# Kernel optimization log

Measured on AMD Instinct MI355X. Metric: run time of the kernel, lower is better.

## Reference

```python
import jax, jax.numpy as jnp
import numpy as np

EPS = 1e-8  # matches F.cosine_similarity default eps


def setup_inputs() -> dict:
    key = jax.random.key(0)
    k1, k2, k3 = jax.random.split(key, 3)
    B, C, H, W = 16, 256, 64, 64
    n_e = 1024
    z = jax.random.normal(k1, (B, C, H, W), dtype=jnp.float32)
    gt = jax.random.normal(k2, (B, C, H, W), dtype=jnp.float32)
    codebook = jax.random.normal(k3, (n_e, C), dtype=jnp.float32)
    return {"z": z, "gt": gt, "codebook": codebook}


def _sq_dist(x, cb):
    return (jnp.sum(x * x, axis=1, keepdims=True)
            + jnp.sum(cb * cb, axis=1)
            - 2.0 * x @ cb.T)


def reference(z, gt, codebook):
    B, C, H, W = z.shape
    # permute to (B,H,W,C) then flatten to (N, e_dim)
    zf = jnp.transpose(z, (0, 2, 3, 1)).reshape(-1, C)
    gf = jnp.transpose(gt, (0, 2, 3, 1)).reshape(-1, C)

    idx = jnp.argmin(_sq_dist(zf, codebook), axis=1)       # [N]
    idx_gt = jnp.argmin(_sq_dist(gf, codebook), axis=1)    # [N]

    # one-hot @ codebook == direct gather
    z_q = codebook[idx].reshape(B, H, W, C)
    z_q_gt = codebook[idx_gt].reshape(B, H, W, C)

    # F.cosine_similarity(z_q_gt, z_q, dim=1) on (B,H,W,C): reduces over H -> (B,W,C)
    num = jnp.sum(z_q_gt * z_q, axis=1)
    nx = jnp.maximum(jnp.sqrt(jnp.sum(z_q_gt * z_q_gt, axis=1)), EPS)
    ny = jnp.maximum(jnp.sqrt(jnp.sum(z_q * z_q, axis=1)), EPS)
    cosine_score = num / (nx * ny)                         # (B, W, C)

    return cosine_score, idx_gt[:, None], idx[:, None]
```

## Files before the change

kernel.cpp:

```cpp
#include <hip/hip_runtime.h>

typedef _Float16 f16x8 __attribute__((ext_vector_type(8)));
typedef float f32x4 __attribute__((ext_vector_type(4)));

#define CDIM 256
#define NE 1024
#define HW 4096
#define CHW 1048576
#define OUT_COS 262144
#define N_PIX 65536
#define NT 32
#define TAU 0.1f


__global__ void prep_kernel(const float* __restrict__ cb,
                            _Float16* __restrict__ hi,
                            float* __restrict__ c2f,
                            double* __restrict__ c2d) {
    int code = blockIdx.x;
    int lane = threadIdx.x;
    int t = code >> 5, sub = (code >> 4) & 1, n = code & 15;
    const float* row = cb + code * CDIM;
    double s = 0.0;
    #pragma unroll
    for (int i = 0; i < 4; ++i) {
        int d = i * 64 + lane;
        float x = row[d];
        s += (double)x * (double)x;
        int f = d >> 5, q = (d >> 3) & 3, r = d & 7;
        hi[(size_t)t * 8192 + sub * 4096 + f * 512 + q * 128 + n * 8 + r] =
            (_Float16)x;
    }
    #pragma unroll
    for (int off = 32; off > 0; off >>= 1)
        s += __shfl_down(s, off, 64);
    if (lane == 0) { c2f[code] = (float)(0.5 * s); c2d[code] = 0.5 * s; }
}

__device__ __forceinline__ void gl_lds16(const _Float16* g, _Float16* l) {
    __builtin_amdgcn_global_load_lds(
        (const __attribute__((address_space(1))) unsigned int*)g,
        (__attribute__((address_space(3))) unsigned int*)l, 16, 0, 0);
}

__attribute__((amdgpu_waves_per_eu(2, 2)))
__launch_bounds__(256)
__global__ void argmin_kernel(const float* __restrict__ Z,
                              const float* __restrict__ GT,
                              const _Float16* __restrict__ ghi,
                              const float* __restrict__ cb,
                              const float* __restrict__ c2f,
                              const double* __restrict__ c2d,
                              float* __restrict__ out_z,
                              float* __restrict__ out_gt) {
    __shared__ __align__(16) _Float16 lbuf[2][8192];
    __shared__ int cand_lds[4][64];
    __shared__ float c2s[NE];
    const int wave = threadIdx.x >> 6;
    const int lane = threadIdx.x & 63;
    const int l15 = lane & 15;
    const int quad = lane >> 4;
    const int half = blockIdx.x >> 8;
    const float* X = half ? GT : Z;
    float* out_idx = half ? out_gt : out_z;
    const int p0 = (blockIdx.x & 255) * 256;

    #pragma unroll
    for (int i = 0; i < 4; ++i)
        c2s[i * 256 + threadIdx.x] = c2f[i * 256 + threadIdx.x];

    f16x8 nah[4][8];
    #pragma unroll
    for (int g = 0; g < 4; ++g) {
        const int p = p0 + wave * 64 + g * 16 + l15;
        const float* xbase = X + (size_t)(p >> 12) * CHW + (p & 4095);
        #pragma unroll
        for (int f = 0; f < 8; ++f) {
            #pragma unroll
            for (int j = 0; j < 8; ++j) {
                int d = f * 32 + quad * 8 + j;
                nah[g][f][j] = -(_Float16)xbase[(size_t)d * HW];
            }
        }
    }

    int b1[4][4], b2[4][4];
    #pragma unroll
    for (int g = 0; g < 4; ++g)
        #pragma unroll
        for (int r = 0; r < 4; ++r) { b1[g][r] = 0x7fffffff; b2[g][r] = 0x7fffffff; }

    auto stage = [&](int b, int t) {
        #pragma unroll
        for (int i = 0; i < 4; ++i) {
            const int c = wave * 4 + i;
            gl_lds16(ghi + (size_t)t * 8192 + c * 512 + lane * 8, &lbuf[b][c * 512]);
        }
    };

    stage(0, 0);
    __syncthreads();

    for (int t = 0; t < NT; ++t) {
        const int cur = t & 1;
        if (t < NT - 1) stage(cur ^ 1, t + 1);

        #pragma unroll
        for (int sub = 0; sub < 2; ++sub) {
            const int n = t * 32 + sub * 16 + l15;
            const float c2 = c2s[n];
            f32x4 acc[4];
            #pragma unroll
            for (int g = 0; g < 4; ++g)
                acc[g] = (f32x4){c2, c2, c2, c2};

            #pragma unroll
            for (int f = 0; f < 8; ++f) {
                f16x8 bh = *(const f16x8*)&lbuf[cur][sub * 4096 + f * 512 + lane * 8];
                acc[0] = __builtin_amdgcn_mfma_f32_16x16x32_f16(nah[0][f], bh, acc[0], 0, 0, 0);
                acc[1] = __builtin_amdgcn_mfma_f32_16x16x32_f16(nah[1][f], bh, acc[1], 0, 0, 0);
                acc[2] = __builtin_amdgcn_mfma_f32_16x16x32_f16(nah[2][f], bh, acc[2], 0, 0, 0);
                acc[3] = __builtin_amdgcn_mfma_f32_16x16x32_f16(nah[3][f], bh, acc[3], 0, 0, 0);
            }

            #pragma unroll
            for (int g = 0; g < 4; ++g) {
                #pragma unroll
                for (int r = 0; r < 4; ++r) {
                    int k = (__float_as_int(acc[g][r]) & 0xFFFFFC00) | n;
                    int mx = max(b1[g][r], k);
                    b2[g][r] = min(b2[g][r], mx);
                    b1[g][r] = min(b1[g][r], k);
                }
            }
        }
        __syncthreads();
    }

    #pragma unroll
    for (int g = 0; g < 4; ++g) {
        #pragma unroll
        for (int r = 0; r < 4; ++r) {
            int x1 = b1[g][r], x2 = b2[g][r];
            #pragma unroll
            for (int off = 8; off > 0; off >>= 1) {
                int o1 = __shfl_xor(x1, off, 64);
                int o2 = __shfl_xor(x2, off, 64);
                int tt = max(x1, o1);
                x2 = min(min(x2, o2), tt);
                x1 = min(x1, o1);
            }
            if (l15 == 0) {
                const int i1 = x1 & 1023, i2 = x2 & 1023;
                const float s1 = __int_as_float(x1 & 0xFFFFFC00);
                const float s2 = __int_as_float(x2 & 0xFFFFFC00);
                const int row = quad * 4 + r;
                const int slot = g * 16 + row;
                const bool flag = (s2 - s1) < TAU;
                cand_lds[wave][slot] = i1 | (i2 << 10) | (flag ? (1 << 20) : 0);
                if (!flag) out_idx[p0 + wave * 64 + slot] = (float)i1;
            }
        }
    }

    const int info = cand_lds[wave][lane];
    if (info & (1 << 20)) {
        const int i1 = info & 1023, i2 = (info >> 10) & 1023;
        const int p = p0 + wave * 64 + lane;
        const float* xb = X + (size_t)(p >> 12) * CHW + (p & 4095);
        const float* r1 = cb + (size_t)i1 * CDIM;
        const float* r2 = cb + (size_t)i2 * CDIM;
        double d1 = 0.0, d2 = 0.0;
        #pragma unroll 4
        for (int d = 0; d < CDIM; d += 4) {
            float x0 = xb[(size_t)(d + 0) * HW];
            float x1v = xb[(size_t)(d + 1) * HW];
            float x2v = xb[(size_t)(d + 2) * HW];
            float x3v = xb[(size_t)(d + 3) * HW];
            const float4 v1 = *(const float4*)(r1 + d);
            const float4 v2 = *(const float4*)(r2 + d);
            d1 += (double)x0 * v1.x + (double)x1v * v1.y
                + (double)x2v * v1.z + (double)x3v * v1.w;
            d2 += (double)x0 * v2.x + (double)x1v * v2.y
                + (double)x2v * v2.z + (double)x3v * v2.w;
        }
        const double dd1 = c2d[i1] - d1;
        const double dd2 = c2d[i2] - d2;
        const int bi = (dd2 < dd1 || (dd2 == dd1 && i2 < i1)) ? i2 : i1;
        out_idx[p] = (float)bi;
    }
}

__global__ void cosine_kernel(const float* __restrict__ cb,
                              const float* __restrict__ idx_z_f,
                              const float* __restrict__ idx_gt_f,
                              float* __restrict__ out_cos) {
    __shared__ int s_ig[64], s_iq[64];
    const int bw = blockIdx.x;
    const int c = threadIdx.x;
    const int b = bw >> 6, w = bw & 63;
    if (c < 64) {
        s_ig[c] = (int)idx_gt_f[b * 4096 + c * 64 + w];
    } else if (c < 128) {
        int h = c - 64;
        s_iq[h] = (int)idx_z_f[b * 4096 + h * 64 + w];
    }
    __syncthreads();
    float num = 0.f, sa = 0.f, sb = 0.f;
    #pragma unroll 1
    for (int h = 0; h < 64; h += 4) {
        float av[4], bv[4];
        #pragma unroll
        for (int u = 0; u < 4; ++u) {
            av[u] = cb[s_ig[h + u] * CDIM + c];
            bv[u] = cb[s_iq[h + u] * CDIM + c];
        }
        #pragma unroll
        for (int u = 0; u < 4; ++u) {
            num += av[u] * bv[u];
            sa += av[u] * av[u];
            sb += bv[u] * bv[u];
        }
    }
    const float nx = fmaxf(sqrtf(sa), 1e-8f);
    const float ny = fmaxf(sqrtf(sb), 1e-8f);
    out_cos[bw * CDIM + c] = num / (nx * ny);
}

extern "C" void kernel_launch(void* const* d_in, const int* in_sizes, int n_in,
                              void* d_out, int out_size, void* d_ws, size_t ws_size,
                              hipStream_t stream) {
    const float* z  = (const float*)d_in[0];
    const float* gt = (const float*)d_in[1];
    const float* cb = (const float*)d_in[2];
    float* out = (float*)d_out;

    _Float16* hi = (_Float16*)d_ws;
    float*  c2f = (float*)((char*)d_ws + 512 * 1024);
    double* c2d = (double*)((char*)d_ws + 516 * 1024);

    float* out_cos    = out;
    float* out_idx_gt = out + OUT_COS;
    float* out_idx_z  = out + OUT_COS + N_PIX;

    prep_kernel<<<NE, 64, 0, stream>>>(cb, hi, c2f, c2d);
    argmin_kernel<<<512, 256, 0, stream>>>(z, gt, hi, cb, c2f, c2d,
                                           out_idx_z, out_idx_gt);
    cosine_kernel<<<1024, 256, 0, stream>>>(cb, out_idx_z, out_idx_gt, out_cos);
}
```

Measured before the change: 250.1 us.

## Stage input activations through padded LDS with async double-buffered global-to-LDS loads

Activation loading into MFMA A-fragments now uses double-buffered global_load_lds copies into padded LDS rows, one 32-channel slice at a time, aliased onto the codebook buffer. Previously each lane did 256 scalar strided global loads, so loads were poorly coalesced and latency-bound. The padded row stride is meant to avoid LDS bank conflicts during the transposing reads. The launch attribute also changes from waves_per_eu(2,2) to launch_bounds(256,2), which may alter register allocation.

```diff
diff --git a/kernel.cpp b/kernel.cpp
--- a/kernel.cpp
+++ b/kernel.cpp
@@ -11,6 +11,9 @@
 #define N_PIX 65536
 #define NT 32
 #define TAU 0.1f
+
+#define XROW_DW 260
+#define XS_DW   (32 * XROW_DW)
 
 
 __global__ void prep_kernel(const float* __restrict__ cb,
@@ -37,14 +40,13 @@
     if (lane == 0) { c2f[code] = (float)(0.5 * s); c2d[code] = 0.5 * s; }
 }
 
-__device__ __forceinline__ void gl_lds16(const _Float16* g, _Float16* l) {
+__device__ __forceinline__ void gl_lds16(const void* g, void* l) {
     __builtin_amdgcn_global_load_lds(
         (const __attribute__((address_space(1))) unsigned int*)g,
         (__attribute__((address_space(3))) unsigned int*)l, 16, 0, 0);
 }
 
-__attribute__((amdgpu_waves_per_eu(2, 2)))
-__launch_bounds__(256)
+__launch_bounds__(256, 2)
 __global__ void argmin_kernel(const float* __restrict__ Z,
                               const float* __restrict__ GT,
                               const _Float16* __restrict__ ghi,
@@ -53,9 +55,12 @@
                               const double* __restrict__ c2d,
                               float* __restrict__ out_z,
                               float* __restrict__ out_gt) {
-    __shared__ __align__(16) _Float16 lbuf[2][8192];
-    __shared__ int cand_lds[4][64];
-    __shared__ float c2s[NE];
+    __shared__ __align__(16) char smem[2 * 33280 + 4096 + 1024];
+    float*    xs   = (float*)smem;
+    _Float16* lbuf = (_Float16*)smem;
+    float*    c2s  = (float*)(smem + 66560);
+    int*      cand = (int*)(smem + 70656);
+
     const int wave = threadIdx.x >> 6;
     const int lane = threadIdx.x & 63;
     const int l15 = lane & 15;
@@ -69,20 +74,38 @@
     for (int i = 0; i < 4; ++i)
         c2s[i * 256 + threadIdx.x] = c2f[i * 256 + threadIdx.x];
 
+    const float* xsrc = X + (size_t)(p0 >> 12) * CHW + (p0 & 4095);
+
+    auto stage_x = [&](int b, int fr) {
+        #pragma unroll
+        for (int i = 0; i < 8; ++i) {
+            const int row = wave * 8 + i;
+            const int d = fr * 32 + row;
+            gl_lds16(xsrc + (size_t)d * HW + lane * 4,
+                     xs + b * XS_DW + row * XROW_DW);
+        }
+    };
+
     f16x8 nah[4][8];
-    #pragma unroll
-    for (int g = 0; g < 4; ++g) {
-        const int p = p0 + wave * 64 + g * 16 + l15;
-        const float* xbase = X + (size_t)(p >> 12) * CHW + (p & 4095);
-        #pragma unroll
-        for (int f = 0; f < 8; ++f) {
-            #pragma unroll
-            for (int j = 0; j < 8; ++j) {
-                int d = f * 32 + quad * 8 + j;
-                nah[g][f][j] = -(_Float16)xbase[(size_t)d * HW];
-            }
-        }
-    }
+    stage_x(0, 0);
+    int xb = 0;
+    #pragma unroll
+    for (int f = 0; f < 8; ++f) {
+        __syncthreads();
+        if (f < 7) stage_x(xb ^ 1, f + 1);
+        const float* xsb = xs + xb * XS_DW;
+        const int abase = quad * 8 * XROW_DW + wave * 64 + l15;
+        #pragma unroll
+        for (int g = 0; g < 4; ++g) {
+            f16x8 t;
+            #pragma unroll
+            for (int j = 0; j < 8; ++j)
+                t[j] = -(_Float16)xsb[abase + j * XROW_DW + g * 16];
+            nah[g][f] = t;
+        }
+        xb ^= 1;
+    }
+    __syncthreads();
 
     int b1[4][4], b2[4][4];
     #pragma unroll
@@ -94,7 +117,8 @@
         #pragma unroll
         for (int i = 0; i < 4; ++i) {
             const int c = wave * 4 + i;
-            gl_lds16(ghi + (size_t)t * 8192 + c * 512 + lane * 8, &lbuf[b][c * 512]);
+            gl_lds16(ghi + (size_t)t * 8192 + c * 512 + lane * 8,
+                     lbuf + b * 8192 + c * 512);
         }
     };
 
@@ -116,7 +140,7 @@
 
             #pragma unroll
             for (int f = 0; f < 8; ++f) {
-                f16x8 bh = *(const f16x8*)&lbuf[cur][sub * 4096 + f * 512 + lane * 8];
+                f16x8 bh = *(const f16x8*)&lbuf[cur * 8192 + sub * 4096 + f * 512 + lane * 8];
                 acc[0] = __builtin_amdgcn_mfma_f32_16x16x32_f16(nah[0][f], bh, acc[0], 0, 0, 0);
                 acc[1] = __builtin_amdgcn_mfma_f32_16x16x32_f16(nah[1][f], bh, acc[1], 0, 0, 0);
                 acc[2] = __builtin_amdgcn_mfma_f32_16x16x32_f16(nah[2][f], bh, acc[2], 0, 0, 0);
@@ -157,26 +181,26 @@
                 const int row = quad * 4 + r;
                 const int slot = g * 16 + row;
                 const bool flag = (s2 - s1) < TAU;
-                cand_lds[wave][slot] = i1 | (i2 << 10) | (flag ? (1 << 20) : 0);
+                cand[wave * 64 + slot] = i1 | (i2 << 10) | (flag ? (1 << 20) : 0);
                 if (!flag) out_idx[p0 + wave * 64 + slot] = (float)i1;
             }
         }
     }
 
-    const int info = cand_lds[wave][lane];
+    const int info = cand[wave * 64 + lane];
     if (info & (1 << 20)) {
         const int i1 = info & 1023, i2 = (info >> 10) & 1023;
         const int p = p0 + wave * 64 + lane;
-        const float* xb = X + (size_t)(p >> 12) * CHW + (p & 4095);
+        const float* xb2 = X + (size_t)(p >> 12) * CHW + (p & 4095);
         const float* r1 = cb + (size_t)i1 * CDIM;
         const float* r2 = cb + (size_t)i2 * CDIM;
         double d1 = 0.0, d2 = 0.0;
         #pragma unroll 4
         for (int d = 0; d < CDIM; d += 4) {
-            float x0 = xb[(size_t)(d + 0) * HW];
-            float x1v = xb[(size_t)(d + 1) * HW];
-            float x2v = xb[(size_t)(d + 2) * HW];
-            float x3v = xb[(size_t)(d + 3) * HW];
+            float x0 = xb2[(size_t)(d + 0) * HW];
+            float x1v = xb2[(size_t)(d + 1) * HW];
+            float x2v = xb2[(size_t)(d + 2) * HW];
+            float x3v = xb2[(size_t)(d + 3) * HW];
             const float4 v1 = *(const float4*)(r1 + d);
             const float4 v2 = *(const float4*)(r2 + d);
             d1 += (double)x0 * v1.x + (double)x1v * v1.y
```

New measurement: 232.5 us. 7.0% less time.
